# Optimization experiments

Hardware: AMD Instinct MI355X
Metric: run time of the kernel (lower is better)

The kernel has to match this reference:

```python
import jax, jax.numpy as jnp
import numpy as np

MCMC_STEPS = 30
STEP_SIZE = 0.01
NOISE = 0.005
COEF_REG = 0.001
EPS = 1e-12  # torch F.normalize eps


def l2norm(x):
    # F.normalize(x, p=2, dim=-1): x / max(||x||, eps)
    return x / jnp.maximum(jnp.linalg.norm(x, axis=-1, keepdims=True), EPS)


def energy_matrix(vid, txt):
    # all-pairs cossim energy, avg-pooled over frames -> [bst, bsv]
    vn = l2norm(vid)  # [b, f, d]
    tn = l2norm(txt)  # [a, d]
    return -jnp.mean(jnp.einsum('bfd,ad->abf', vn, tn), axis=-1)


def energy_diag(vid, txt):
    # paired cossim energy, avg-pooled over frames -> [a]
    vn = l2norm(vid)  # [a, f, d]
    tn = l2norm(txt)  # [a, d]
    return -jnp.mean(jnp.einsum('afd,ad->af', vn, tn), axis=-1)


def _e_sum(v, t):
    return energy_diag(v, t).sum()

_energy_grad = jax.grad(_e_sum, argnums=(0, 1))


def mcmc_sample(vid_init, txt_init, key):
    # sample(): uniform [-1,1] init (first-call path), then Langevin steps.
    # torch detaches at every step, so the whole sampler is non-differentiable.
    v = 2.0 * jax.lax.stop_gradient(vid_init) - 1.0
    t = 2.0 * jax.lax.stop_gradient(txt_init) - 1.0

    def step(carry, k):
        v, t = carry
        gv, gt = _energy_grad(v, t)
        kv, kt = jax.random.split(k)
        v = v - STEP_SIZE * gv + NOISE * jax.random.normal(kv, v.shape, v.dtype)
        t = t - STEP_SIZE * gt + NOISE * jax.random.normal(kt, t.shape, t.dtype)
        return (v, t), None

    (v, t), _ = jax.lax.scan(step, (v, t), jax.random.split(key, MCMC_STEPS))
    return jax.lax.stop_gradient(v), jax.lax.stop_gradient(t)


def ebm_loss(pos_mean, neg_mean, pos_sq_mean, neg_sq_mean):
    return pos_mean - neg_mean + COEF_REG * (pos_sq_mean + neg_sq_mean)


def setup_inputs() -> dict:
    key = jax.random.key(0)
    k1, k2, k3, k4 = jax.random.split(key, 4)
    B, F, D = 1024, 12, 512
    return {
        'vid': jax.random.normal(k1, (B, F, D), jnp.float32),
        'txt': jax.random.normal(k2, (B, D), jnp.float32),
        'vid_init': jax.random.uniform(k3, (B, F, D), jnp.float32),
        'txt_init': jax.random.uniform(k4, (B, D), jnp.float32),
    }


def reference(vid, txt, vid_init, txt_init):
    B = vid.shape[0]
    E = energy_matrix(vid, txt)  # [B, B]
    pos = jnp.diagonal(E)        # [B]
    # off-diagonal stats without materializing a boolean-mask gather
    n_neg = B * (B - 1)
    neg_mean = (E.sum() - pos.sum()) / n_neg
    neg_sq_mean = ((E * E).sum() - (pos * pos).sum()) / n_neg
    loss1 = ebm_loss(pos.mean(), neg_mean, jnp.mean(pos * pos), neg_sq_mean)

    vid_s, txt_s = mcmc_sample(vid_init, txt_init, jax.random.key(42))
    e_s = energy_diag(vid_s, txt_s)  # [B]
    loss2 = ebm_loss(pos.mean(), e_s.mean(), jnp.mean(pos * pos), jnp.mean(e_s * e_s))

    return (loss1 + loss2) / 2.0
```

## Files before the change

### kernel.cpp

```cpp
#include <hip/hip_runtime.h>
#include <cstdint>

namespace {

constexpr int kB = 1024;
constexpr int kF = 12;
constexpr int kD = 512;
constexpr int kNT = kB * kD;

#define TF_ROUND(r) { x0 += x1; x1 = (x1 << (r)) | (x1 >> (32 - (r))); x1 ^= x0; }

__host__ __device__ inline void tf2x32(uint32_t k0, uint32_t k1,
                                       uint32_t c0, uint32_t c1,
                                       uint32_t& o0, uint32_t& o1) {
  uint32_t ks2 = k0 ^ k1 ^ 0x1BD11BDAu;
  uint32_t x0 = c0 + k0;
  uint32_t x1 = c1 + k1;
  TF_ROUND(13) TF_ROUND(15) TF_ROUND(26) TF_ROUND(6)
  x0 += k1;  x1 += ks2 + 1u;
  TF_ROUND(17) TF_ROUND(29) TF_ROUND(16) TF_ROUND(24)
  x0 += ks2; x1 += k0 + 2u;
  TF_ROUND(13) TF_ROUND(15) TF_ROUND(26) TF_ROUND(6)
  x0 += k0;  x1 += k1 + 3u;
  TF_ROUND(17) TF_ROUND(29) TF_ROUND(16) TF_ROUND(24)
  x0 += k1;  x1 += ks2 + 4u;
  TF_ROUND(13) TF_ROUND(15) TF_ROUND(26) TF_ROUND(6)
  x0 += ks2; x1 += k0 + 5u;
  o0 = x0; o1 = x1;
}

__device__ __forceinline__ uint32_t rbits0(uint32_t k0, uint32_t k1,
                                           uint32_t ks2, uint32_t i) {
#define RR(r) { x0 += x1; x1 = __builtin_rotateleft32(x1, r); x1 ^= x0; }
  uint32_t x0 = k0;
  uint32_t x1 = i + k1;
  RR(13) RR(15) RR(26) RR(6)
  x0 += k1;  x1 += ks2 + 1u;
  RR(17) RR(29) RR(16) RR(24)
  x0 += ks2; x1 += k0 + 2u;
  RR(13) RR(15) RR(26) RR(6)
  x0 += k0;  x1 += k1 + 3u;
  RR(17) RR(29) RR(16) RR(24)
  x0 += k1;  x1 += ks2 + 4u;
  RR(13) RR(15) RR(26) RR(6)
  x0 += ks2; x1 += k0 + 5u;
  return x0 ^ x1;
#undef RR
}

__device__ __forceinline__ float fast_log2(float x) {
#if __has_builtin(__builtin_amdgcn_logf)
  return __builtin_amdgcn_logf(x);
#else
  return __log2f(x);
#endif
}

__device__ __forceinline__ float fast_sqrt(float x) {
#if __has_builtin(__builtin_amdgcn_sqrtf)
  return __builtin_amdgcn_sqrtf(x);
#else
  return sqrtf(x);
#endif
}

__device__ __forceinline__ float rsq_nr(float x) {
#if __has_builtin(__builtin_amdgcn_rsqf)
  float r = __builtin_amdgcn_rsqf(x);
#else
  float r = 1.0f / sqrtf(x);
#endif
  float h = 0.5f * x;
  return r * (1.5f - h * r * r);
}

__device__ __forceinline__ float normpx(uint32_t bits) {
  float f = __uint_as_float((bits >> 9) | 0x3F800000u) - 1.0f;
  const float lo = __uint_as_float(0xBF7FFFFFu);
  float u = fmaxf(lo, fmaf(f, 2.0f, lo));
  float y = fmaf(-u, u, 1.0f);
  float w = -0.69314718055994531f * fast_log2(y);
  float wa = w - 2.5f;
  float p = 2.81022636e-08f;
  p = fmaf(p, wa, 3.43273939e-07f);
  p = fmaf(p, wa, -3.5233877e-06f);
  p = fmaf(p, wa, -4.39150654e-06f);
  p = fmaf(p, wa, 0.00021858087f);
  p = fmaf(p, wa, -0.00125372503f);
  p = fmaf(p, wa, -0.00417768164f);
  p = fmaf(p, wa, 0.246640727f);
  p = fmaf(p, wa, 1.50140941f);
  if (__builtin_expect(__any(w >= 5.0f), 0)) {
    float wb = fast_sqrt(w) - 3.0f;
    float pb = -0.000200214257f;
    pb = fmaf(pb, wb, 0.000100950558f);
    pb = fmaf(pb, wb, 0.00134934322f);
    pb = fmaf(pb, wb, -0.00367342844f);
    pb = fmaf(pb, wb, 0.00573950773f);
    pb = fmaf(pb, wb, -0.0076224613f);
    pb = fmaf(pb, wb, 0.00943887047f);
    pb = fmaf(pb, wb, 1.00167406f);
    pb = fmaf(pb, wb, 2.83297682f);
    p = (w < 5.0f) ? p : pb;
  }
  return p * u;
}

__device__ __forceinline__ float swz_add(float x) {
  x += __int_as_float(__builtin_amdgcn_ds_swizzle(__float_as_int(x), 0x041F));
  x += __int_as_float(__builtin_amdgcn_ds_swizzle(__float_as_int(x), 0x081F));
  x += __int_as_float(__builtin_amdgcn_ds_swizzle(__float_as_int(x), 0x101F));
  x += __int_as_float(__builtin_amdgcn_ds_swizzle(__float_as_int(x), 0x201F));
  x += __int_as_float(__builtin_amdgcn_ds_swizzle(__float_as_int(x), 0x401F));
  return x;
}

__device__ __forceinline__ float breduce(float x, float* s4) {
#pragma unroll
  for (int o = 32; o; o >>= 1) x += __shfl_xor(x, o);
  const int w = threadIdx.x >> 6;
  if ((threadIdx.x & 63) == 0) s4[w] = x;
  __syncthreads();
  float r = s4[0] + s4[1] + s4[2] + s4[3];
  __syncthreads();
  return r;
}

struct KeyChain { uint32_t k[120]; };

__global__ __launch_bounds__(256) void k_vidmean(const float* __restrict__ vid,
                                                 float* __restrict__ vm) {
  __shared__ float s4[4];
  const int b = blockIdx.x, tid = threadIdx.x;
  float a0 = 0.f, a1 = 0.f;
  for (int f = 0; f < kF; ++f) {
    const float* row = vid + (b * kF + f) * kD;
    float x0 = row[tid], x1 = row[tid + 256];
    float nn = breduce(x0 * x0 + x1 * x1, s4);
    float n = fmaxf(sqrtf(nn), 1e-12f);
    a0 += x0 / n;
    a1 += x1 / n;
  }
  vm[b * kD + tid] = a0 / 12.0f;
  vm[b * kD + tid + 256] = a1 / 12.0f;
}

__global__ __launch_bounds__(256) void k_txtpos(const float* __restrict__ txt,
                                                const float* __restrict__ vm,
                                                float* __restrict__ tn,
                                                float* __restrict__ posbuf) {
  __shared__ float s4[4];
  const int a = blockIdx.x, tid = threadIdx.x;
  float x0 = txt[a * kD + tid], x1 = txt[a * kD + tid + 256];
  float nn = breduce(x0 * x0 + x1 * x1, s4);
  float n = fmaxf(sqrtf(nn), 1e-12f);
  float y0 = x0 / n, y1 = x1 / n;
  tn[a * kD + tid] = y0;
  tn[a * kD + tid + 256] = y1;
  float d = y0 * vm[a * kD + tid] + y1 * vm[a * kD + tid + 256];
  float dot = breduce(d, s4);
  if (tid == 0) posbuf[a] = dot;
}

__global__ __launch_bounds__(256) void k_egemm(const float* __restrict__ A,
                                               const float* __restrict__ Bm,
                                               double* __restrict__ acc) {
  __shared__ float As[64][65];
  __shared__ float Bs[64][65];
  __shared__ double rs[8];
  const int tid = threadIdx.x;
  const int aBase = blockIdx.y * 64;
  const int bBase = blockIdx.x * 64;
  const int tx = tid & 15, ty = tid >> 4;
  float c[4][4];
#pragma unroll
  for (int i = 0; i < 4; ++i)
#pragma unroll
    for (int j = 0; j < 4; ++j) c[i][j] = 0.f;

  for (int kk = 0; kk < kD; kk += 64) {
#pragma unroll
    for (int l = 0; l < 16; ++l) {
      int li = l * 256 + tid;
      int row = li >> 6, col = li & 63;
      As[row][col] = A[(aBase + row) * kD + kk + col];
      Bs[row][col] = Bm[(bBase + row) * kD + kk + col];
    }
    __syncthreads();
#pragma unroll 4
    for (int k = 0; k < 64; ++k) {
      float a0 = As[ty][k], a1 = As[ty + 16][k], a2 = As[ty + 32][k], a3 = As[ty + 48][k];
      float b0 = Bs[tx][k], b1 = Bs[tx + 16][k], b2 = Bs[tx + 32][k], b3 = Bs[tx + 48][k];
      c[0][0] = fmaf(a0, b0, c[0][0]); c[0][1] = fmaf(a0, b1, c[0][1]);
      c[0][2] = fmaf(a0, b2, c[0][2]); c[0][3] = fmaf(a0, b3, c[0][3]);
      c[1][0] = fmaf(a1, b0, c[1][0]); c[1][1] = fmaf(a1, b1, c[1][1]);
      c[1][2] = fmaf(a1, b2, c[1][2]); c[1][3] = fmaf(a1, b3, c[1][3]);
      c[2][0] = fmaf(a2, b0, c[2][0]); c[2][1] = fmaf(a2, b1, c[2][1]);
      c[2][2] = fmaf(a2, b2, c[2][2]); c[2][3] = fmaf(a2, b3, c[2][3]);
      c[3][0] = fmaf(a3, b0, c[3][0]); c[3][1] = fmaf(a3, b1, c[3][1]);
      c[3][2] = fmaf(a3, b2, c[3][2]); c[3][3] = fmaf(a3, b3, c[3][3]);
    }
    __syncthreads();
  }
  double s1 = 0.0, s2 = 0.0;
#pragma unroll
  for (int i = 0; i < 4; ++i)
#pragma unroll
    for (int j = 0; j < 4; ++j) {
      double cd = (double)c[i][j];
      s1 += cd;
      s2 += cd * cd;
    }
#pragma unroll
  for (int o = 32; o; o >>= 1) {
    s1 += __shfl_xor(s1, o);
    s2 += __shfl_xor(s2, o);
  }
  const int wid = tid >> 6;
  if ((tid & 63) == 0) { rs[wid] = s1; rs[wid + 4] = s2; }
  __syncthreads();
  if (tid == 0) {
    atomicAdd(&acc[0], rs[0] + rs[1] + rs[2] + rs[3]);
    atomicAdd(&acc[1], rs[4] + rs[5] + rs[6] + rs[7]);
  }
}

__global__ __launch_bounds__(256) void k_mcmc(const float* __restrict__ vinit,
                                              const float* __restrict__ tinit,
                                              float* __restrict__ esbuf,
                                              KeyChain K) {
  __shared__ float part[8][26];
  __shared__ float tot[26];
  const int a = blockIdx.x, tid = threadIdx.x;
  const uint32_t vbase = (uint32_t)a * (uint32_t)(kF * kD) + (uint32_t)tid;
  const uint32_t tbase = (uint32_t)a * (uint32_t)kD + (uint32_t)tid;
  float v0[kF], v1[kF];
#pragma unroll
  for (int f = 0; f < kF; ++f) {
    v0[f] = 2.0f * vinit[vbase + f * kD] - 1.0f;
    v1[f] = 2.0f * vinit[vbase + f * kD + 256] - 1.0f;
  }
  float t0 = 2.0f * tinit[tbase] - 1.0f;
  float t1 = 2.0f * tinit[tbase + 256] - 1.0f;

  const float CZ = 0.0070710678118654755f;

  for (int j = 0; j <= 30; ++j) {
    {
      float r = swz_add(t0 * t0 + t1 * t1);
      if ((tid & 31) == 0) part[tid >> 5][0] = r;
    }
#pragma unroll
    for (int f = 0; f < kF; ++f) {
      float rv = swz_add(v0[f] * v0[f] + v1[f] * v1[f]);
      float rt = swz_add(v0[f] * t0 + v1[f] * t1);
      if ((tid & 31) == 0) {
        part[tid >> 5][1 + f] = rv;
        part[tid >> 5][13 + f] = rt;
      }
    }
    __syncthreads();
    if (tid < 25) {
      float s = 0.f;
#pragma unroll
      for (int r = 0; r < 8; ++r) s += part[r][tid];
      tot[tid] = s;
    }
    __syncthreads();

    float minv = rsq_nr(tot[0]);

    if (j == 30) {
      float se = 0.f;
#pragma unroll
      for (int f = 0; f < kF; ++f)
        se += tot[13 + f] * rsq_nr(tot[1 + f]) * minv;
      if (tid == 0) esbuf[a] = -se * (1.0f / 12.0f);
      break;
    }

    const uint32_t kv0 = K.k[4 * j + 0], kv1 = K.k[4 * j + 1];
    const uint32_t kt0 = K.k[4 * j + 2], kt1 = K.k[4 * j + 3];
    const uint32_t ksv = kv0 ^ kv1 ^ 0x1BD11BDAu;
    const uint32_t kst = kt0 ^ kt1 ^ 0x1BD11BDAu;
    float w0 = t0 * minv, w1 = t1 * minv;
    float q0 = 0.f, q1 = 0.f, qw = 0.f;
#pragma unroll
    for (int f = 0; f < kF; ++f) {
      float ninv = rsq_nr(tot[1 + f]);
      float s = tot[13 + f] * ninv * minv;
      qw += s;
      float u0 = v0[f] * ninv, u1 = v1[f] * ninv;
      q0 += u0; q1 += u1;
      float h = ninv * (0.01f / 12.0f);
      const uint32_t iv = vbase + (uint32_t)(f * kD);
      float p0 = normpx(rbits0(kv0, kv1, ksv, iv));
      float p1 = normpx(rbits0(kv0, kv1, ksv, iv + 256u));
      v0[f] = fmaf(CZ, p0, fmaf(h, fmaf(-s, u0, w0), v0[f]));
      v1[f] = fmaf(CZ, p1, fmaf(h, fmaf(-s, u1, w1), v1[f]));
    }
    q0 *= (1.0f / 12.0f); q1 *= (1.0f / 12.0f); qw *= (1.0f / 12.0f);
    float ht = 0.01f * minv;
    float p0 = normpx(rbits0(kt0, kt1, kst, tbase));
    float p1 = normpx(rbits0(kt0, kt1, kst, tbase + 256u));
    t0 = fmaf(CZ, p0, fmaf(ht, fmaf(-qw, w0, q0), t0));
    t1 = fmaf(CZ, p1, fmaf(ht, fmaf(-qw, w1, q1), t1));
  }
}

__global__ __launch_bounds__(256) void k_fin(const double* __restrict__ acc,
                                             const float* __restrict__ posbuf,
                                             const float* __restrict__ esbuf,
                                             float* __restrict__ out) {
  __shared__ double sd[4][4];
  const int tid = threadIdx.x;
  double pd = 0, pd2 = 0, pe = 0, pe2 = 0;
  for (int i = tid; i < kB; i += 256) {
    double d = (double)posbuf[i];
    double e = (double)esbuf[i];
    pd += d; pd2 += d * d;
    pe += e; pe2 += e * e;
  }
#pragma unroll
  for (int o = 32; o; o >>= 1) {
    pd += __shfl_xor(pd, o);  pd2 += __shfl_xor(pd2, o);
    pe += __shfl_xor(pe, o);  pe2 += __shfl_xor(pe2, o);
  }
  const int w = tid >> 6;
  if ((tid & 63) == 0) { sd[w][0] = pd; sd[w][1] = pd2; sd[w][2] = pe; sd[w][3] = pe2; }
  __syncthreads();
  if (tid == 0) {
    double sumdot  = sd[0][0] + sd[1][0] + sd[2][0] + sd[3][0];
    double sumdot2 = sd[0][1] + sd[1][1] + sd[2][1] + sd[3][1];
    double es      = sd[0][2] + sd[1][2] + sd[2][2] + sd[3][2];
    double es2     = sd[0][3] + sd[1][3] + sd[2][3] + sd[3][3];
    double S1 = acc[0], S2 = acc[1];
    const double nn = 1024.0 * 1023.0;
    double pos_mean = -sumdot / 1024.0;
    double neg_mean = (-S1 + sumdot) / nn;
    double pos_sq   = sumdot2 / 1024.0;
    double neg_sq   = (S2 - sumdot2) / nn;
    double loss1 = pos_mean - neg_mean + 0.001 * (pos_sq + neg_sq);
    double loss2 = pos_mean - es / 1024.0 + 0.001 * (pos_sq + es2 / 1024.0);
    out[0] = (float)(0.5 * (loss1 + loss2));
  }
}

}

extern "C" void kernel_launch(void* const* d_in, const int* in_sizes, int n_in,
                              void* d_out, int out_size, void* d_ws, size_t ws_size,
                              hipStream_t stream) {
  (void)in_sizes; (void)n_in; (void)out_size; (void)ws_size;
  const float* vid   = (const float*)d_in[0];
  const float* txt   = (const float*)d_in[1];
  const float* vinit = (const float*)d_in[2];
  const float* tinit = (const float*)d_in[3];
  float* out = (float*)d_out;

  char* ws = (char*)d_ws;
  double* acc   = (double*)ws;
  float* posbuf = (float*)(ws + 256);
  float* esbuf  = posbuf + kB;
  float* tn     = esbuf + kB;
  float* vm     = tn + kNT;

  hipMemsetAsync(acc, 0, 64, stream);

  k_vidmean<<<kB, 256, 0, stream>>>(vid, vm);
  k_txtpos<<<kB, 256, 0, stream>>>(txt, vm, tn, posbuf);
  k_egemm<<<dim3(16, 16), 256, 0, stream>>>(tn, vm, acc);

  KeyChain K;
  for (uint32_t j = 0; j < 30; ++j) {
    uint32_t s0, s1, kv0, kv1, kt0, kt1;
    tf2x32(0u, 42u, 0u, j, s0, s1);
    tf2x32(s0, s1, 0u, 0u, kv0, kv1);
    tf2x32(s0, s1, 0u, 1u, kt0, kt1);
    K.k[4 * j + 0] = kv0; K.k[4 * j + 1] = kv1;
    K.k[4 * j + 2] = kt0; K.k[4 * j + 3] = kt1;
  }

  k_mcmc<<<kB, 256, 0, stream>>>(vinit, tinit, esbuf, K);

  k_fin<<<1, 256, 0, stream>>>(acc, posbuf, esbuf, out);
}
```

Baseline: 572.8 us.

## Use 512 threads per MCMC block with one element per thread

The Langevin sampler kernel now launches 512 threads per sample instead of 256, so each thread owns one column of the 512-wide feature vector instead of two. The goal is to halve per-thread serial work (RNG and normal transforms) and register pressure and to raise occupancy, at the cost of 16 partial rows in the shared-memory reduction instead of 8. The uniform-to-normal conversion also builds the uniform value with an int-to-float fmaf instead of bit tricks plus a clamp, which could change rounding slightly at the edges of the range.

Measured after the change: 593.8 us. 1.04x slower.

```diff
diff --git a/kernel.cpp b/kernel.cpp
--- a/kernel.cpp
+++ b/kernel.cpp
@@ -75,9 +75,8 @@
 }
 
 __device__ __forceinline__ float normpx(uint32_t bits) {
-  float f = __uint_as_float((bits >> 9) | 0x3F800000u) - 1.0f;
   const float lo = __uint_as_float(0xBF7FFFFFu);
-  float u = fmaxf(lo, fmaf(f, 2.0f, lo));
+  float u = fmaf((float)(bits >> 9), 0x1p-22f, lo);
   float y = fmaf(-u, u, 1.0f);
   float w = -0.69314718055994531f * fast_log2(y);
   float wa = w - 2.5f;
@@ -225,35 +224,32 @@
   }
 }
 
-__global__ __launch_bounds__(256) void k_mcmc(const float* __restrict__ vinit,
+__global__ __launch_bounds__(512) void k_mcmc(const float* __restrict__ vinit,
                                               const float* __restrict__ tinit,
                                               float* __restrict__ esbuf,
                                               KeyChain K) {
-  __shared__ float part[8][26];
+  __shared__ float part[16][26];
   __shared__ float tot[26];
   const int a = blockIdx.x, tid = threadIdx.x;
   const uint32_t vbase = (uint32_t)a * (uint32_t)(kF * kD) + (uint32_t)tid;
   const uint32_t tbase = (uint32_t)a * (uint32_t)kD + (uint32_t)tid;
-  float v0[kF], v1[kF];
-#pragma unroll
-  for (int f = 0; f < kF; ++f) {
+  float v0[kF];
+#pragma unroll
+  for (int f = 0; f < kF; ++f)
     v0[f] = 2.0f * vinit[vbase + f * kD] - 1.0f;
-    v1[f] = 2.0f * vinit[vbase + f * kD + 256] - 1.0f;
-  }
   float t0 = 2.0f * tinit[tbase] - 1.0f;
-  float t1 = 2.0f * tinit[tbase + 256] - 1.0f;
 
   const float CZ = 0.0070710678118654755f;
 
   for (int j = 0; j <= 30; ++j) {
     {
-      float r = swz_add(t0 * t0 + t1 * t1);
+      float r = swz_add(t0 * t0);
       if ((tid & 31) == 0) part[tid >> 5][0] = r;
     }
 #pragma unroll
     for (int f = 0; f < kF; ++f) {
-      float rv = swz_add(v0[f] * v0[f] + v1[f] * v1[f]);
-      float rt = swz_add(v0[f] * t0 + v1[f] * t1);
+      float rv = swz_add(v0[f] * v0[f]);
+      float rt = swz_add(v0[f] * t0);
       if ((tid & 31) == 0) {
         part[tid >> 5][1 + f] = rv;
         part[tid >> 5][13 + f] = rt;
@@ -263,7 +259,7 @@
     if (tid < 25) {
       float s = 0.f;
 #pragma unroll
-      for (int r = 0; r < 8; ++r) s += part[r][tid];
+      for (int r = 0; r < 16; ++r) s += part[r][tid];
       tot[tid] = s;
     }
     __syncthreads();
@@ -283,28 +279,23 @@
     const uint32_t kt0 = K.k[4 * j + 2], kt1 = K.k[4 * j + 3];
     const uint32_t ksv = kv0 ^ kv1 ^ 0x1BD11BDAu;
     const uint32_t kst = kt0 ^ kt1 ^ 0x1BD11BDAu;
-    float w0 = t0 * minv, w1 = t1 * minv;
-    float q0 = 0.f, q1 = 0.f, qw = 0.f;
+    float w0 = t0 * minv;
+    float q0 = 0.f, qw = 0.f;
 #pragma unroll
     for (int f = 0; f < kF; ++f) {
       float ninv = rsq_nr(tot[1 + f]);
       float s = tot[13 + f] * ninv * minv;
       qw += s;
-      float u0 = v0[f] * ninv, u1 = v1[f] * ninv;
-      q0 += u0; q1 += u1;
+      float u0 = v0[f] * ninv;
+      q0 += u0;
       float h = ninv * (0.01f / 12.0f);
-      const uint32_t iv = vbase + (uint32_t)(f * kD);
-      float p0 = normpx(rbits0(kv0, kv1, ksv, iv));
-      float p1 = normpx(rbits0(kv0, kv1, ksv, iv + 256u));
+      float p0 = normpx(rbits0(kv0, kv1, ksv, vbase + (uint32_t)(f * kD)));
       v0[f] = fmaf(CZ, p0, fmaf(h, fmaf(-s, u0, w0), v0[f]));
-      v1[f] = fmaf(CZ, p1, fmaf(h, fmaf(-s, u1, w1), v1[f]));
-    }
-    q0 *= (1.0f / 12.0f); q1 *= (1.0f / 12.0f); qw *= (1.0f / 12.0f);
+    }
+    q0 *= (1.0f / 12.0f); qw *= (1.0f / 12.0f);
     float ht = 0.01f * minv;
     float p0 = normpx(rbits0(kt0, kt1, kst, tbase));
-    float p1 = normpx(rbits0(kt0, kt1, kst, tbase + 256u));
     t0 = fmaf(CZ, p0, fmaf(ht, fmaf(-qw, w0, q0), t0));
-    t1 = fmaf(CZ, p1, fmaf(ht, fmaf(-qw, w1, q1), t1));
   }
 }
 
@@ -381,7 +372,7 @@
     K.k[4 * j + 2] = kt0; K.k[4 * j + 3] = kt1;
   }
 
-  k_mcmc<<<kB, 256, 0, stream>>>(vinit, tinit, esbuf, K);
+  k_mcmc<<<kB, 512, 0, stream>>>(vinit, tinit, esbuf, K);
 
   k_fin<<<1, 256, 0, stream>>>(acc, posbuf, esbuf, out);
 }
```
